# Kernel tuning notes

Measured on AMD Instinct MI355X. Metric: run time of the kernel, lower is better.

Reference implementation:

```python
import jax, jax.numpy as jnp
import numpy as np

B, K, H, W = 8, 1024, 24, 24
C = H * W            # in_channels = 576
NH = 6               # hardcoded num_heads
HD = C // NH         # 96


def setup_inputs() -> dict:
    key = jax.random.key(0)
    ks = jax.random.split(key, 8)
    s = 1.0 / np.sqrt(C)
    return {
        "input1": jax.random.normal(ks[0], (B, K, H, W), jnp.float32),
        "input2": jax.random.normal(ks[1], (B, K, H, W), jnp.float32),
        "Wq": jax.random.uniform(ks[2], (C, C), jnp.float32, -s, s),
        "bq": jax.random.uniform(ks[3], (C,), jnp.float32, -s, s),
        "Wk": jax.random.uniform(ks[4], (C, C), jnp.float32, -s, s),
        "bk": jax.random.uniform(ks[5], (C,), jnp.float32, -s, s),
        "Wv": jax.random.uniform(ks[6], (C, C), jnp.float32, -s, s),
        "bv": jax.random.uniform(ks[7], (C,), jnp.float32, -s, s),
    }


def reference(input1, input2, Wq, bq, Wk, bk, Wv, bv):
    b, k, h, w = input1.shape
    c = h * w
    x1 = input1.reshape(b, k, c)
    x2 = input2.reshape(b, k, c)
    # torch nn.Linear: y = x @ W^T + b
    q = x1 @ Wq.T + bq                      # [b, k, c]
    kk = x2 @ Wk.T + bk
    v = x2 @ Wv.T + bv
    # torch .view scrambles: [b, k, c] -> [b, NH, c//NH, k] (row-major reshape)
    q = q.reshape(b, NH, c // NH, k)
    kk = kk.reshape(b, NH, c // NH, k)
    v = v.reshape(b, NH, c // NH, k)
    # scores = q^T k over head-dim; NOTE: no 1/sqrt(d) scaling in original
    scores = jnp.einsum('bhdq,bhdk->bhqk', q, kk)   # [b, NH, k, k]
    weights = jax.nn.softmax(scores, axis=-1)
    # context = value @ weights^T -> [b, NH, hd, k]
    ctx = jnp.einsum('bhdk,bhqk->bhdq', v, weights)
    return ctx.reshape(b, k, h, w)
```

## Files before the change

### kernel.cpp

```cpp
#include <hip/hip_runtime.h>
#include <cmath>

#define BATCH 8
#define KDIM  1024
#define CH    576
#define NHEAD 6
#define HDIM  96

typedef _Float16 f16;
typedef f16 f16x4 __attribute__((ext_vector_type(4)));
typedef f16 f16x8 __attribute__((ext_vector_type(8)));
typedef float f32x16 __attribute__((ext_vector_type(16)));
typedef unsigned int u32;

#define PSZ  (BATCH * KDIM * CH)
#define WSZ  (CH * CH)

__device__ inline f32x16 zero16() {
    f32x16 z;
#pragma unroll
    for (int r = 0; r < 16; ++r) z[r] = 0.f;
    return z;
}

__global__ __launch_bounds__(256) void convert_kernel(
    const float* __restrict__ x1, const float* __restrict__ x2,
    const float* __restrict__ Wq, const float* __restrict__ Wk,
    const float* __restrict__ Wv,
    f16* __restrict__ x1h, f16* __restrict__ x2h, f16* __restrict__ wh)
{
    const int y = blockIdx.y;
    int idx = blockIdx.x * 256 + threadIdx.x;
    const float* src;
    f16* dst;
    if (y == 0) {
        if (idx >= PSZ / 8) return;
        src = x1; dst = x1h;
    } else if (y == 1) {
        if (idx >= PSZ / 8) return;
        src = x2; dst = x2h;
    } else {
        if (idx >= 3 * WSZ / 8) return;
        int seg = idx / (WSZ / 8);
        src = (seg == 0) ? Wq : (seg == 1) ? Wk : Wv;
        dst = wh + seg * WSZ;
        idx -= seg * (WSZ / 8);
        if (y > 2) return;
    }
    float4 u0 = ((const float4*)src)[2 * idx];
    float4 u1 = ((const float4*)src)[2 * idx + 1];
    f16x8 hv;
    hv[0] = (f16)u0.x; hv[1] = (f16)u0.y; hv[2] = (f16)u0.z; hv[3] = (f16)u0.w;
    hv[4] = (f16)u1.x; hv[5] = (f16)u1.y; hv[6] = (f16)u1.z; hv[7] = (f16)u1.w;
    ((f16x8*)dst)[idx] = hv;
}

__global__ __launch_bounds__(256) void proj_kernel(
    const f16* __restrict__ x1h, const f16* __restrict__ x2h,
    const f16* __restrict__ wh,
    const float* __restrict__ bq, const float* __restrict__ bk,
    const float* __restrict__ bv,
    f16* __restrict__ qf, f16* __restrict__ kf, f16* __restrict__ vf)
{
    const int z = blockIdx.z;
    const f16* A     = (z == 0) ? x1h : x2h;
    const f16* W     = wh + z * WSZ;
    const float* bias = (z == 0) ? bq : (z == 1) ? bk : bv;
    f16* dst          = (z == 0) ? qf : (z == 1) ? kf : vf;

    __shared__ f16 As[128 * 72];
    __shared__ f16 Ws[192 * 72];

    const int tid = threadIdx.x;
    const int lane = tid & 63, w = tid >> 6;
    const int l31 = lane & 31, half = lane >> 5;
    const int nBase = blockIdx.x * 192;
    const int mBase = blockIdx.y * 128;

    f32x16 acc[6] = {zero16(), zero16(), zero16(), zero16(), zero16(), zero16()};

    for (int k0 = 0; k0 < CH; k0 += 64) {
        __syncthreads();
#pragma unroll
        for (int r = 0; r < 4; ++r) {
            int idx = r * 256 + tid;
            int row = idx >> 3, ch = idx & 7;
            *(f16x8*)&As[row * 72 + ch * 8] =
                *(const f16x8*)&A[(size_t)(mBase + row) * CH + k0 + ch * 8];
        }
#pragma unroll
        for (int r = 0; r < 6; ++r) {
            int idx = r * 256 + tid;
            int row = idx >> 3, ch = idx & 7;
            *(f16x8*)&Ws[row * 72 + ch * 8] =
                *(const f16x8*)&W[(size_t)(nBase + row) * CH + k0 + ch * 8];
        }
        __syncthreads();
#pragma unroll
        for (int ks = 0; ks < 4; ++ks) {
            f16x8 a = *(const f16x8*)&As[(32 * w + l31) * 72 + 16 * ks + 8 * half];
#pragma unroll
            for (int nt = 0; nt < 6; ++nt) {
                f16x8 bfr = *(const f16x8*)&Ws[(32 * nt + l31) * 72 + 16 * ks + 8 * half];
                acc[nt] = __builtin_amdgcn_mfma_f32_32x32x16_f16(a, bfr, acc[nt], 0, 0, 0);
            }
        }
    }

#pragma unroll
    for (int nt = 0; nt < 6; ++nt) {
        int n = nBase + 32 * nt + l31;
        float bsv = bias[n];
#pragma unroll
        for (int r = 0; r < 16; ++r) {
            int m = mBase + 32 * w + (r & 3) + 8 * (r >> 2) + 4 * half;
            dst[(size_t)m * CH + n] = (f16)(acc[nt][r] + bsv);
        }
    }
}

__global__ __launch_bounds__(256) void transpose_qk(
    const f16* __restrict__ qf, const f16* __restrict__ kf,
    f16* __restrict__ QT, f16* __restrict__ KT)
{
    const int tt = blockIdx.x;
    const int bh = blockIdx.y;
    const f16* src = blockIdx.z ? kf : qf;
    f16* dst = blockIdx.z ? KT : QT;

    __shared__ f16 Ts[96 * 72];

    const int tid = threadIdx.x;
    const int rowbase = (bh / NHEAD) * CH + (bh % NHEAD) * HDIM;

#pragma unroll
    for (int r = 0; r < 3; ++r) {
        int idx = r * 256 + tid;
        int d = idx >> 3, g = idx & 7;
        *(f16x8*)&Ts[d * 72 + g * 8] =
            *(const f16x8*)&src[(size_t)(rowbase + d) * KDIM + tt * 64 + g * 8];
    }
    __syncthreads();
#pragma unroll
    for (int r = 0; r < 3; ++r) {
        int idx = r * 256 + tid;
        int t = idx & 63, dg = idx >> 6;
        f16x8 v;
#pragma unroll
        for (int u = 0; u < 8; ++u) v[u] = Ts[(dg * 8 + u) * 72 + t];
        *(f16x8*)&dst[((size_t)bh * KDIM + tt * 64 + t) * HDIM + dg * 8] = v;
    }
}

__global__ __launch_bounds__(256, 3) void attn_kernel(
    const f16* __restrict__ qT, const f16* __restrict__ kT,
    const f16* __restrict__ vf, float* __restrict__ out)
{
    __shared__ __align__(16) char smem[27136];
    f16* Ks = (f16*)smem;
    f16* Vs = (f16*)(smem + 13312);
    f16* Qs = Ks;

    const int qt = blockIdx.x;
    const int h  = blockIdx.y;
    const int b  = blockIdx.z;
    const int bh = b * NHEAD + h;

    const int tid = threadIdx.x;
    const int lane = tid & 63, w = tid >> 6;
    const int ih = w & 1, jg = w >> 1;
    const int l31 = lane & 31, half = lane >> 5;
    const int iw = 32 * ih;

    const f16* Qbase = qT + ((size_t)bh * KDIM + qt * 64) * HDIM;
    const f16* Kbase = kT + (size_t)bh * KDIM * HDIM;
    const f16* Vbase = vf + ((size_t)b * CH + (size_t)h * HDIM) * KDIM;

    int kt[3], kg[3], vd[3], vg[3];
#pragma unroll
    for (int r = 0; r < 3; ++r) {
        int idx = r * 256 + tid;
        kt[r] = idx / 12; kg[r] = idx % 12;
        vd[r] = idx >> 3; vg[r] = idx & 7;
    }

#pragma unroll
    for (int r = 0; r < 3; ++r)
        *(f16x8*)&Qs[kt[r] * 104 + kg[r] * 8] =
            *(const f16x8*)&Qbase[kt[r] * 96 + kg[r] * 8];
    __syncthreads();
    f16x8 qfr[6];
#pragma unroll
    for (int ks = 0; ks < 6; ++ks)
        qfr[ks] = *(const f16x8*)&Qs[(iw + l31) * 104 + 16 * ks + 8 * half];

    f16x8 kreg[3], vreg[3];
#pragma unroll
    for (int r = 0; r < 3; ++r) {
        kreg[r] = *(const f16x8*)&Kbase[(size_t)kt[r] * HDIM + kg[r] * 8];
        vreg[r] = *(const f16x8*)&Vbase[(size_t)vd[r] * KDIM + vg[r] * 8];
    }

    float m_run = -INFINITY, l_run = 0.f;
    f32x16 Oacc[3] = {zero16(), zero16(), zero16()};

    for (int jt = 0; jt < KDIM; jt += 64) {
        __syncthreads();
#pragma unroll
        for (int r = 0; r < 3; ++r) {
            *(f16x8*)&Ks[kt[r] * 104 + kg[r] * 8] = kreg[r];
            *(f16x8*)&Vs[vd[r] * 72 + vg[r] * 8]  = vreg[r];
        }
        __syncthreads();
        if (jt + 64 < KDIM) {
#pragma unroll
            for (int r = 0; r < 3; ++r) {
                kreg[r] = *(const f16x8*)&Kbase[(size_t)(jt + 64 + kt[r]) * HDIM + kg[r] * 8];
                vreg[r] = *(const f16x8*)&Vbase[(size_t)vd[r] * KDIM + jt + 64 + vg[r] * 8];
            }
        }

        f32x16 s0 = zero16();
#pragma unroll
        for (int ks = 0; ks < 6; ++ks) {
            f16x8 ak = *(const f16x8*)&Ks[(32 * jg + l31) * 104 + 16 * ks + 8 * half];
            s0 = __builtin_amdgcn_mfma_f32_32x32x16_f16(ak, qfr[ks], s0, 0, 0, 0);
        }

        float mx = -INFINITY;
#pragma unroll
        for (int r = 0; r < 16; ++r) mx = fmaxf(mx, s0[r]);
        mx = fmaxf(mx, __shfl_xor(mx, 32));
        float mnew = fmaxf(m_run, mx);
        float alpha = __expf(m_run - mnew);
        m_run = mnew;
        float sum = 0.f;
        f16x4 pq[4];
#pragma unroll
        for (int r = 0; r < 16; ++r) {
            float e = __expf(s0[r] - mnew);
            sum += e;
            pq[r >> 2][r & 3] = (f16)e;
        }
        sum += __shfl_xor(sum, 32);
        l_run = alpha * l_run + sum;

        if (__any(alpha != 1.0f)) {
#pragma unroll
            for (int t = 0; t < 3; ++t)
#pragma unroll
                for (int r = 0; r < 16; ++r) Oacc[t][r] *= alpha;
        }

#pragma unroll
        for (int kc = 0; kc < 2; ++kc) {
            union { f16x4 h; u32 u[2]; } snd, rcv, keep;
            keep.h = half ? pq[2 * kc + 1] : pq[2 * kc];
            snd.h  = half ? pq[2 * kc]     : pq[2 * kc + 1];
            rcv.u[0] = __shfl_xor((int)snd.u[0], 32);
            rcv.u[1] = __shfl_xor((int)snd.u[1], 32);
            f16x8 bp;
            if (half == 0) {
#pragma unroll
                for (int v = 0; v < 4; ++v) { bp[v] = keep.h[v]; bp[4 + v] = rcv.h[v]; }
            } else {
#pragma unroll
                for (int v = 0; v < 4; ++v) { bp[v] = rcv.h[v]; bp[4 + v] = keep.h[v]; }
            }
            int jo = 32 * jg + 16 * kc + 8 * half;
#pragma unroll
            for (int t = 0; t < 3; ++t) {
                f16x8 av = *(const f16x8*)&Vs[(32 * t + l31) * 72 + jo];
                Oacc[t] = __builtin_amdgcn_mfma_f32_32x32x16_f16(av, bp, Oacc[t], 0, 0, 0);
            }
        }
    }

    __syncthreads();
    float* Oscr = (float*)smem;
    float* mScr = (float*)(smem + 25344);
    float* lScr = (float*)(smem + 25600);
    if (jg == 1) {
        if (half == 0) { mScr[iw + l31] = m_run; lScr[iw + l31] = l_run; }
        float* od = Oscr + ih * 3168;
#pragma unroll
        for (int t = 0; t < 3; ++t)
#pragma unroll
            for (int r = 0; r < 16; ++r) {
                int d = 32 * t + (r & 3) + 8 * (r >> 2) + 4 * half;
                od[d * 33 + l31] = Oacc[t][r];
            }
    }
    __syncthreads();
    if (jg == 0) {
        float m1 = mScr[iw + l31], l1 = lScr[iw + l31];
        float mstar = fmaxf(m_run, m1);
        float a0 = __expf(m_run - mstar), a1 = __expf(m1 - mstar);
        float linv = 1.0f / (l_run * a0 + l1 * a1);
        const float* od = Oscr + ih * 3168;
        float* obase = out + ((size_t)b * CH + (size_t)h * HDIM) * KDIM
                           + qt * 64 + iw + l31;
#pragma unroll
        for (int t = 0; t < 3; ++t)
#pragma unroll
            for (int r = 0; r < 16; ++r) {
                int d = 32 * t + (r & 3) + 8 * (r >> 2) + 4 * half;
                obase[(size_t)d * KDIM] =
                    (Oacc[t][r] * a0 + od[d * 33 + l31] * a1) * linv;
            }
    }
}

extern "C" void kernel_launch(void* const* d_in, const int* in_sizes, int n_in,
                              void* d_out, int out_size, void* d_ws, size_t ws_size,
                              hipStream_t stream)
{
    const float* x1 = (const float*)d_in[0];
    const float* x2 = (const float*)d_in[1];
    const float* Wq = (const float*)d_in[2];
    const float* bq = (const float*)d_in[3];
    const float* Wk = (const float*)d_in[4];
    const float* bk = (const float*)d_in[5];
    const float* Wv = (const float*)d_in[6];
    const float* bv = (const float*)d_in[7];
    float* out = (float*)d_out;

    const size_t P = PSZ;
    f16* x1h = (f16*)d_ws;
    f16* x2h = x1h + P;
    f16* qf  = x2h + P;
    f16* kf  = qf + P;
    f16* vf  = kf + P;
    f16* wh  = vf + P;
    f16* QT  = x1h;
    f16* KT  = x2h;

    dim3 cgrid((P / 8 + 255) / 256, 3);
    convert_kernel<<<cgrid, 256, 0, stream>>>(x1, x2, Wq, Wk, Wv, x1h, x2h, wh);

    dim3 pgrid(CH / 192, (BATCH * KDIM) / 128, 3);
    proj_kernel<<<pgrid, 256, 0, stream>>>(x1h, x2h, wh, bq, bk, bv, qf, kf, vf);

    dim3 tgrid(KDIM / 64, BATCH * NHEAD, 2);
    transpose_qk<<<tgrid, 256, 0, stream>>>(qf, kf, QT, KT);

    dim3 agrid(KDIM / 64, NHEAD, BATCH);
    attn_kernel<<<agrid, 256, 0, stream>>>(QT, KT, vf, out);
}
```

Measured before the change: 175.9 us.

## Shrink projection M tile, split warps 2x2, and register-prefetch next K slice

The projection GEMM tile goes from 128x192 to 64x192. Warps are now arranged 2x2, each computing 32x96, so they hold 3 accumulators instead of 6. The next K slice is loaded into registers while the MFMAs run on the current shared-memory tile, and launch_bounds now requests 4 blocks per SM for occupancy. The aim is to hide global load latency and double the grid, at the cost of less reuse of the W tile per block. A dead early-return was also removed from the convert kernel.

```diff
diff --git a/kernel.cpp b/kernel.cpp
--- a/kernel.cpp
+++ b/kernel.cpp
@@ -45,7 +45,6 @@
         src = (seg == 0) ? Wq : (seg == 1) ? Wk : Wv;
         dst = wh + seg * WSZ;
         idx -= seg * (WSZ / 8);
-        if (y > 2) return;
     }
     float4 u0 = ((const float4*)src)[2 * idx];
     float4 u1 = ((const float4*)src)[2 * idx + 1];
@@ -55,7 +54,7 @@
     ((f16x8*)dst)[idx] = hv;
 }
 
-__global__ __launch_bounds__(256) void proj_kernel(
+__global__ __launch_bounds__(256, 4) void proj_kernel(
     const f16* __restrict__ x1h, const f16* __restrict__ x2h,
     const f16* __restrict__ wh,
     const float* __restrict__ bq, const float* __restrict__ bk,
@@ -63,57 +62,78 @@
     f16* __restrict__ qf, f16* __restrict__ kf, f16* __restrict__ vf)
 {
     const int z = blockIdx.z;
-    const f16* A     = (z == 0) ? x1h : x2h;
-    const f16* W     = wh + z * WSZ;
+    const f16* A      = (z == 0) ? x1h : x2h;
+    const f16* W      = wh + z * WSZ;
     const float* bias = (z == 0) ? bq : (z == 1) ? bk : bv;
     f16* dst          = (z == 0) ? qf : (z == 1) ? kf : vf;
 
-    __shared__ f16 As[128 * 72];
+    __shared__ f16 As[64 * 72];
     __shared__ f16 Ws[192 * 72];
 
     const int tid = threadIdx.x;
     const int lane = tid & 63, w = tid >> 6;
     const int l31 = lane & 31, half = lane >> 5;
+    const int mw = 32 * (w & 1), nh = 96 * (w >> 1);
     const int nBase = blockIdx.x * 192;
-    const int mBase = blockIdx.y * 128;
-
-    f32x16 acc[6] = {zero16(), zero16(), zero16(), zero16(), zero16(), zero16()};
+    const int mBase = blockIdx.y * 64;
+
+    int arow[2], ach[2], wrow[6], wch[6];
+#pragma unroll
+    for (int r = 0; r < 2; ++r) {
+        int idx = r * 256 + tid;
+        arow[r] = idx >> 3; ach[r] = idx & 7;
+    }
+#pragma unroll
+    for (int r = 0; r < 6; ++r) {
+        int idx = r * 256 + tid;
+        wrow[r] = idx >> 3; wch[r] = idx & 7;
+    }
+
+    f16x8 aP[2], wP[6];
+#pragma unroll
+    for (int r = 0; r < 2; ++r)
+        aP[r] = *(const f16x8*)&A[(size_t)(mBase + arow[r]) * CH + ach[r] * 8];
+#pragma unroll
+    for (int r = 0; r < 6; ++r)
+        wP[r] = *(const f16x8*)&W[(size_t)(nBase + wrow[r]) * CH + wch[r] * 8];
+
+    f32x16 acc[3] = {zero16(), zero16(), zero16()};
 
     for (int k0 = 0; k0 < CH; k0 += 64) {
         __syncthreads();
 #pragma unroll
-        for (int r = 0; r < 4; ++r) {
-            int idx = r * 256 + tid;
-            int row = idx >> 3, ch = idx & 7;
-            *(f16x8*)&As[row * 72 + ch * 8] =
-                *(const f16x8*)&A[(size_t)(mBase + row) * CH + k0 + ch * 8];
-        }
-#pragma unroll
-        for (int r = 0; r < 6; ++r) {
-            int idx = r * 256 + tid;
-            int row = idx >> 3, ch = idx & 7;
-            *(f16x8*)&Ws[row * 72 + ch * 8] =
-                *(const f16x8*)&W[(size_t)(nBase + row) * CH + k0 + ch * 8];
-        }
+        for (int r = 0; r < 2; ++r)
+            *(f16x8*)&As[arow[r] * 72 + ach[r] * 8] = aP[r];
+#pragma unroll
+        for (int r = 0; r < 6; ++r)
+            *(f16x8*)&Ws[wrow[r] * 72 + wch[r] * 8] = wP[r];
         __syncthreads();
+        if (k0 + 64 < CH) {
+#pragma unroll
+            for (int r = 0; r < 2; ++r)
+                aP[r] = *(const f16x8*)&A[(size_t)(mBase + arow[r]) * CH + k0 + 64 + ach[r] * 8];
+#pragma unroll
+            for (int r = 0; r < 6; ++r)
+                wP[r] = *(const f16x8*)&W[(size_t)(nBase + wrow[r]) * CH + k0 + 64 + wch[r] * 8];
+        }
 #pragma unroll
         for (int ks = 0; ks < 4; ++ks) {
-            f16x8 a = *(const f16x8*)&As[(32 * w + l31) * 72 + 16 * ks + 8 * half];
-#pragma unroll
-            for (int nt = 0; nt < 6; ++nt) {
-                f16x8 bfr = *(const f16x8*)&Ws[(32 * nt + l31) * 72 + 16 * ks + 8 * half];
+            f16x8 a = *(const f16x8*)&As[(mw + l31) * 72 + 16 * ks + 8 * half];
+#pragma unroll
+            for (int nt = 0; nt < 3; ++nt) {
+                f16x8 bfr = *(const f16x8*)&Ws[(nh + 32 * nt + l31) * 72 + 16 * ks + 8 * half];
                 acc[nt] = __builtin_amdgcn_mfma_f32_32x32x16_f16(a, bfr, acc[nt], 0, 0, 0);
             }
         }
     }
 
 #pragma unroll
-    for (int nt = 0; nt < 6; ++nt) {
-        int n = nBase + 32 * nt + l31;
+    for (int nt = 0; nt < 3; ++nt) {
+        int n = nBase + nh + 32 * nt + l31;
         float bsv = bias[n];
 #pragma unroll
         for (int r = 0; r < 16; ++r) {
-            int m = mBase + 32 * w + (r & 3) + 8 * (r >> 2) + 4 * half;
+            int m = mBase + mw + (r & 3) + 8 * (r >> 2) + 4 * half;
             dst[(size_t)m * CH + n] = (f16)(acc[nt][r] + bsv);
         }
     }
@@ -338,7 +358,7 @@
     dim3 cgrid((P / 8 + 255) / 256, 3);
     convert_kernel<<<cgrid, 256, 0, stream>>>(x1, x2, Wq, Wk, Wv, x1h, x2h, wh);
 
-    dim3 pgrid(CH / 192, (BATCH * KDIM) / 128, 3);
+    dim3 pgrid(CH / 192, (BATCH * KDIM) / 64, 3);
     proj_kernel<<<pgrid, 256, 0, stream>>>(x1h, x2h, wh, bq, bk, bv, qf, kf, vf);
 
     dim3 tgrid(KDIM / 64, BATCH * NHEAD, 2);
```

Result: no change. 175.3 us (-0.3%).
